# Optimization experiments

Hardware: AMD Instinct MI355X
Metric: run time of the kernel (lower is better)

Reference implementation:

```python
import jax, jax.numpy as jnp
import numpy as np
import math

B, W, BINS, BANDS = 2, 2048, 1024, 8  # cropsize == W
HEAD = BINS // BANDS


def setup_inputs() -> dict:
    key = jax.random.key(0)
    ks = jax.random.split(key, 10)
    s = 1.0 / math.sqrt(BINS)
    return {
        "x": jax.random.normal(ks[0], (B, W, BINS), jnp.float32),
        "Wq": jax.random.normal(ks[1], (BINS, BINS), jnp.float32) * s,
        "bq": jax.random.normal(ks[2], (BINS,), jnp.float32) * s,
        "Wk": jax.random.normal(ks[3], (BINS, BINS), jnp.float32) * s,
        "bk": jax.random.normal(ks[4], (BINS,), jnp.float32) * s,
        "Wv": jax.random.normal(ks[5], (BINS, BINS), jnp.float32) * s,
        "bv": jax.random.normal(ks[6], (BINS,), jnp.float32) * s,
        "Wo": jax.random.normal(ks[7], (BINS, BINS), jnp.float32) * s,
        "bo": jax.random.normal(ks[8], (BINS,), jnp.float32) * s,
        "er": jax.random.normal(ks[9], (HEAD, W), jnp.float32) * s,  # [bins//num_bands, cropsize]
    }


def reference(x, Wq, bq, Wk, bk, Wv, bv, Wo, bo, er):
    b, w, h = x.shape
    n = BANDS
    # projections -> [b, n, w, head]
    q = (x @ Wq.T + bq).reshape(b, w, n, -1).transpose(0, 2, 1, 3)
    k = (x @ Wk.T + bk).reshape(b, w, n, -1).transpose(0, 2, 1, 3)
    v = (x @ Wv.T + bv).reshape(b, w, n, -1).transpose(0, 2, 1, 3)
    # relative position bias via skew trick: [b, n, w, cropsize]
    qer = jnp.einsum('bnwd,dc->bnwc', q, er)
    p = jnp.pad(qer, ((0, 0), (0, 0), (0, 0), (1, 0)))  # pad left of last dim
    p = jnp.swapaxes(p, 2, 3)[:, :, 1:, :]              # [b, n, w, w]
    a = (jnp.einsum('bnqd,bnkd->bnqk', q, k) + p) / math.sqrt(h)
    attn = jax.nn.softmax(a, axis=-1)
    ctx = jnp.einsum('bnqk,bnkd->bnqd', attn, v).transpose(0, 2, 1, 3).reshape(b, w, h)
    o = ctx @ Wo.T + bo
    return (o, a)
```

## Files before the change

kernel.cpp:

```cpp
#include <hip/hip_runtime.h>

typedef __attribute__((ext_vector_type(8))) __bf16 bf16x8;
typedef __attribute__((ext_vector_type(4))) float f32x4;

__device__ __forceinline__ unsigned short f2bf(float f) {
  __bf16 h = (__bf16)f;
  return __builtin_bit_cast(unsigned short, h);
}

__device__ __forceinline__ f32x4 mfma_bf16(bf16x8 a, bf16x8 b, f32x4 c) {
  return __builtin_amdgcn_mfma_f32_16x16x32_bf16(a, b, c, 0, 0, 0);
}

__device__ __forceinline__ void gload_lds16(const void* g, void* l) {
  __builtin_amdgcn_global_load_lds((const __attribute__((address_space(1))) void*)g,
                                   (__attribute__((address_space(3))) void*)l, 16, 0, 0);
}


__global__ void cvt_f32_bf16(const float* __restrict__ in, unsigned short* __restrict__ out, int n4) {
  int i = blockIdx.x * blockDim.x + threadIdx.x;
  if (i < n4) {
    float4 v = reinterpret_cast<const float4*>(in)[i];
    ushort4 o;
    o.x = f2bf(v.x); o.y = f2bf(v.y); o.z = f2bf(v.z); o.w = f2bf(v.w);
    reinterpret_cast<ushort4*>(out)[i] = o;
  }
}

__global__ void cvt4_f32_bf16(const float* __restrict__ a, const float* __restrict__ b,
                              const float* __restrict__ c, const float* __restrict__ d,
                              unsigned short* __restrict__ oa, unsigned short* __restrict__ ob,
                              unsigned short* __restrict__ oc, unsigned short* __restrict__ od) {
  int i = blockIdx.x * blockDim.x + threadIdx.x;
  int which = i >> 18, j = i & 262143;
  const float* src = (which == 0) ? a : (which == 1) ? b : (which == 2) ? c : d;
  unsigned short* dst = (which == 0) ? oa : (which == 1) ? ob : (which == 2) ? oc : od;
  float4 v = reinterpret_cast<const float4*>(src)[j];
  ushort4 o;
  o.x = f2bf(v.x); o.y = f2bf(v.y); o.z = f2bf(v.z); o.w = f2bf(v.w);
  reinterpret_cast<ushort4*>(dst)[j] = o;
}

__global__ void er_transpose(const float* __restrict__ er, unsigned short* __restrict__ ert) {
  __shared__ float t[32][33];
  int w0 = blockIdx.x * 32, d0 = blockIdx.y * 32;
  int tx = threadIdx.x, ty = threadIdx.y;
#pragma unroll
  for (int i = 0; i < 4; ++i)
    t[ty + i * 8][tx] = er[(size_t)(d0 + ty + i * 8) * 2048 + w0 + tx];
  __syncthreads();
#pragma unroll
  for (int i = 0; i < 4; ++i)
    ert[(size_t)(w0 + ty + i * 8) * 128 + d0 + tx] = f2bf(t[tx][ty + i * 8]);
}


__global__ __launch_bounds__(256, 1) void gemm_qkv3(
    const unsigned short* __restrict__ xb,
    const unsigned short* __restrict__ Wqb, const unsigned short* __restrict__ Wkb,
    const unsigned short* __restrict__ Wvb,
    const float* __restrict__ bq, const float* __restrict__ bk, const float* __restrict__ bvv,
    unsigned short* __restrict__ Qb, unsigned short* __restrict__ Kb,
    unsigned short* __restrict__ Vtb)
{
  __shared__ __align__(16) char lds[131072];

  const int tid = threadIdx.x;
  const int lane = tid & 63, wid = tid >> 6;
  const int lr = lane & 15, lq = lane >> 4;
  const int wr = wid >> 1, wc = wid & 1;
  const int i0 = blockIdx.x * 128, j0 = blockIdx.y * 128;

  f32x4 aQ[4][4] = {}, aK[4][4] = {}, aV[4][4] = {};

  int ldso[4];
  const char *asrc[4], *qsrc[4], *ksrc[4], *vsrc[4];
#pragma unroll
  for (int p = 0; p < 4; ++p) {
    int L = p * 4096 + tid * 16;
    int row = L >> 7, colb = L & 127;
    int sc = colb ^ ((row & 7) << 4);
    ldso[p] = L;
    asrc[p] = (const char*)xb  + (size_t)(i0 + row) * 2048 + sc;
    qsrc[p] = (const char*)Wqb + (size_t)(j0 + row) * 2048 + sc;
    ksrc[p] = (const char*)Wkb + (size_t)(j0 + row) * 2048 + sc;
    vsrc[p] = (const char*)Wvb + (size_t)(j0 + row) * 2048 + sc;
  }

#pragma unroll
  for (int p = 0; p < 4; ++p) gload_lds16(asrc[p], lds + ldso[p]);
#pragma unroll
  for (int p = 0; p < 4; ++p) gload_lds16(qsrc[p], lds + 16384 + ldso[p]);
#pragma unroll
  for (int p = 0; p < 4; ++p) gload_lds16(ksrc[p], lds + 32768 + ldso[p]);
#pragma unroll
  for (int p = 0; p < 4; ++p) gload_lds16(vsrc[p], lds + 49152 + ldso[p]);

  const int swz = (lr & 7) << 4;

  for (int kt = 0; kt < 16; ++kt) {
    char* cb = lds + (kt & 1) * 65536;
    char* nb = lds + ((kt + 1) & 1) * 65536;

    asm volatile("s_waitcnt vmcnt(0)" ::: "memory");
    __builtin_amdgcn_sched_barrier(0);
    __builtin_amdgcn_s_barrier();
    __builtin_amdgcn_sched_barrier(0);

    if (kt < 15) {
      const int k0b = (kt + 1) * 128;
#pragma unroll
      for (int p = 0; p < 4; ++p) gload_lds16(asrc[p] + k0b, nb + ldso[p]);
#pragma unroll
      for (int p = 0; p < 4; ++p) gload_lds16(qsrc[p] + k0b, nb + 16384 + ldso[p]);
#pragma unroll
      for (int p = 0; p < 4; ++p) gload_lds16(ksrc[p] + k0b, nb + 32768 + ldso[p]);
#pragma unroll
      for (int p = 0; p < 4; ++p) gload_lds16(vsrc[p] + k0b, nb + 49152 + ldso[p]);
    }
    __builtin_amdgcn_sched_barrier(0);

#pragma unroll
    for (int kk = 0; kk < 2; ++kk) {
      const int coff = (kk * 64 + lq * 16) ^ swz;
      bf16x8 af[4];
#pragma unroll
      for (int m = 0; m < 4; ++m)
        af[m] = *(const bf16x8*)(cb + (wr * 64 + m * 16 + lr) * 128 + coff);
      bf16x8 bq_[4], bk_[4], bv_[4];
#pragma unroll
      for (int n = 0; n < 4; ++n) {
        const int rb = (wc * 64 + n * 16 + lr) * 128 + coff;
        bq_[n] = *(const bf16x8*)(cb + 16384 + rb);
        bk_[n] = *(const bf16x8*)(cb + 32768 + rb);
        bv_[n] = *(const bf16x8*)(cb + 49152 + rb);
      }
      __builtin_amdgcn_s_setprio(1);
#pragma unroll
      for (int m = 0; m < 4; ++m)
#pragma unroll
        for (int n = 0; n < 4; ++n) {
          aQ[m][n] = mfma_bf16(af[m], bq_[n], aQ[m][n]);
          aK[m][n] = mfma_bf16(af[m], bk_[n], aK[m][n]);
          aV[m][n] = mfma_bf16(af[m], bv_[n], aV[m][n]);
        }
      __builtin_amdgcn_s_setprio(0);
    }
  }

  float vbq[4], vbk[4], vbv[4];
#pragma unroll
  for (int n = 0; n < 4; ++n) {
    int gj = j0 + wc * 64 + n * 16 + lr;
    vbq[n] = bq[gj]; vbk[n] = bk[gj]; vbv[n] = bvv[gj];
  }

#pragma unroll
  for (int m = 0; m < 4; ++m)
#pragma unroll
    for (int n = 0; n < 4; ++n)
#pragma unroll
      for (int r = 0; r < 4; ++r) {
        int gi = i0 + wr * 64 + m * 16 + lq * 4 + r;
        int gj = j0 + wc * 64 + n * 16 + lr;
        Qb[(size_t)gi * 1024 + gj] = f2bf(aQ[m][n][r] + vbq[n]);
        Kb[(size_t)gi * 1024 + gj] = f2bf(aK[m][n][r] + vbk[n]);
      }

  __syncthreads();
  unsigned short* lds16 = (unsigned short*)lds;
#pragma unroll
  for (int m = 0; m < 4; ++m)
#pragma unroll
    for (int n = 0; n < 4; ++n)
#pragma unroll
      for (int r = 0; r < 4; ++r) {
        int il = wr * 64 + m * 16 + lq * 4 + r;
        int jl = wc * 64 + n * 16 + lr;
        lds16[jl * 132 + il] = f2bf(aV[m][n][r] + vbv[n]);
      }
  __syncthreads();
  {
    const int b = i0 >> 11, w0 = i0 & 2047, bd = j0 >> 7;
    for (int idx = tid; idx < 16384; idx += 256) {
      int dl = idx >> 7, wl = idx & 127;
      Vtb[(size_t)((b * 8 + bd) * 128 + dl) * 2048 + w0 + wl] = lds16[dl * 132 + wl];
    }
  }
}


__global__ __launch_bounds__(256, 2) void gemm_bt(
    const unsigned short* __restrict__ A,
    const unsigned short* __restrict__ Bt,
    const float* __restrict__ bias,
    float* __restrict__ C)
{
  __shared__ __align__(16) char base[32768];

  const int tid = threadIdx.x;
  const int lane = tid & 63, wid = tid >> 6;
  const int lr = lane & 15, lq = lane >> 4;
  const int wr = wid >> 1, wc = wid & 1;
  const int i0 = blockIdx.x * 128, j0 = blockIdx.y * 128;

  f32x4 acc[4][4] = {};

  const char* Abase = (const char*)A + (size_t)(i0 + (tid >> 2)) * 2048 + ((tid & 3) << 4);
  const char* Bbase = (const char*)Bt + (size_t)(j0 + (tid >> 2)) * 2048 + ((tid & 3) << 4);

  gload_lds16(Abase,             base + tid * 16);
  gload_lds16(Abase + 64 * 2048, base + 4096 + tid * 16);
  gload_lds16(Bbase,             base + 8192 + tid * 16);
  gload_lds16(Bbase + 64 * 2048, base + 12288 + tid * 16);

  for (int kt = 0; kt < 32; ++kt) {
    char* cbuf = base + (kt & 1) * 16384;
    char* nbuf = base + ((kt + 1) & 1) * 16384;

    asm volatile("s_waitcnt vmcnt(0)" ::: "memory");
    __builtin_amdgcn_sched_barrier(0);
    __builtin_amdgcn_s_barrier();
    __builtin_amdgcn_sched_barrier(0);

    if (kt < 31) {
      const int k0b = (kt + 1) * 64;
      gload_lds16(Abase + k0b,             nbuf + tid * 16);
      gload_lds16(Abase + k0b + 64 * 2048, nbuf + 4096 + tid * 16);
      gload_lds16(Bbase + k0b,             nbuf + 8192 + tid * 16);
      gload_lds16(Bbase + k0b + 64 * 2048, nbuf + 12288 + tid * 16);
    }
    __builtin_amdgcn_sched_barrier(0);

    bf16x8 af[4], bfr[4];
#pragma unroll
    for (int m = 0; m < 4; ++m)
      af[m] = *(const bf16x8*)(cbuf + (wr * 64 + m * 16 + lr) * 64 + lq * 16);
#pragma unroll
    for (int n = 0; n < 4; ++n)
      bfr[n] = *(const bf16x8*)(cbuf + 8192 + (wc * 64 + n * 16 + lr) * 64 + lq * 16);
    __builtin_amdgcn_s_setprio(1);
#pragma unroll
    for (int m = 0; m < 4; ++m)
#pragma unroll
      for (int n = 0; n < 4; ++n)
        acc[m][n] = mfma_bf16(af[m], bfr[n], acc[m][n]);
    __builtin_amdgcn_s_setprio(0);
  }

  float bv[4];
#pragma unroll
  for (int n = 0; n < 4; ++n) bv[n] = bias[j0 + wc * 64 + n * 16 + lr];
#pragma unroll
  for (int m = 0; m < 4; ++m)
#pragma unroll
    for (int n = 0; n < 4; ++n)
#pragma unroll
      for (int r = 0; r < 4; ++r) {
        int gi = i0 + wr * 64 + m * 16 + lq * 4 + r;
        int gj = j0 + wc * 64 + n * 16 + lr;
        C[(size_t)gi * 1024 + gj] = acc[m][n][r] + bv[n];
      }
}


__global__ __launch_bounds__(512) void attn_fused(
    const unsigned short* __restrict__ Qb,
    const unsigned short* __restrict__ Kb,
    const unsigned short* __restrict__ Vt,
    const unsigned short* __restrict__ ErT,
    float* __restrict__ a_out,
    unsigned short* __restrict__ ctx)
{
  __shared__ __align__(16) char Klb[32768];
  __shared__ __align__(16) char Qlb[32768];
  __shared__ __align__(16) char Vlb[32768];
  __shared__ __align__(16) char Plb[32768];

  const int bb = blockIdx.x;
  const int bd = bb & 7, b = bb >> 3;
  const int qi0 = blockIdx.y * 128;
  const int tid = threadIdx.x, wid = tid >> 6, lane = tid & 63;
  const int lr = lane & 15, lq = lane >> 4;

  bf16x8 qf[4], ef[4];
  {
    const unsigned short* Qrow = Qb + (size_t)(b * 2048 + qi0 + wid * 16 + lr) * 1024 + bd * 128;
    const unsigned short* Erow = ErT + (size_t)(qi0 + wid * 16 + lr) * 128;
#pragma unroll
    for (int kk = 0; kk < 4; ++kk) {
      qf[kk] = *(const bf16x8*)(Qrow + kk * 32 + lq * 8);
      ef[kk] = *(const bf16x8*)(Erow + kk * 32 + lq * 8);
    }
  }

  int ldso[4];
  const char *ksrc[4], *qsrc[4], *vsrc[4];
#pragma unroll
  for (int p = 0; p < 4; ++p) {
    int L = p * 8192 + tid * 16;
    int row = L >> 8, cs = L & 255;
    int sc = cs ^ ((row & 7) << 4);
    ldso[p] = L;
    ksrc[p] = (const char*)Kb + ((size_t)(b * 2048 + row) * 1024 + bd * 128) * 2 + sc;
    qsrc[p] = (const char*)Qb + ((size_t)(b * 2048 + row) * 1024 + bd * 128) * 2 + sc;
    vsrc[p] = (const char*)Vt + ((size_t)(bb * 128 + row) * 2048) * 2 + sc;
  }

#pragma unroll
  for (int p = 0; p < 4; ++p) gload_lds16(ksrc[p], Klb + ldso[p]);
#pragma unroll
  for (int p = 0; p < 4; ++p) gload_lds16(qsrc[p], Qlb + ldso[p]);
#pragma unroll
  for (int p = 0; p < 4; ++p) gload_lds16(vsrc[p], Vlb + ldso[p]);
  asm volatile("s_waitcnt vmcnt(0)" ::: "memory");
  __builtin_amdgcn_sched_barrier(0);

  f32x4 oacc[8] = {};
  float M[4], L[4];
#pragma unroll
  for (int r = 0; r < 4; ++r) { M[r] = -1e30f; L[r] = 0.f; }

  float* abase = a_out + (size_t)bb * 2048 * 2048;

  for (int kt = 0; kt < 16; ++kt) {
    const int kj0 = kt * 128;
    const size_t nkq = (size_t)((kt + 1) & 15) * 262144;
    const size_t nv = (size_t)((kt + 1) & 15) * 256;

    asm volatile("s_waitcnt vmcnt(36)" ::: "memory");
    __builtin_amdgcn_sched_barrier(0);
    __builtin_amdgcn_s_barrier();
    __builtin_amdgcn_sched_barrier(0);

    f32x4 sacc[8] = {};
    __builtin_amdgcn_s_setprio(1);
#pragma unroll
    for (int kk = 0; kk < 4; ++kk) {
#pragma unroll
      for (int nf = 0; nf < 8; ++nf) {
        const int row = nf * 16 + lr;
        bf16x8 kf = *(const bf16x8*)(Klb + row * 256 + ((kk * 64 + lq * 16) ^ ((row & 7) << 4)));
        sacc[nf] = mfma_bf16(qf[kk], kf, sacc[nf]);
      }
#pragma unroll
      for (int nf = 0; nf < 8; ++nf) {
        const int row = nf * 16 + lr;
        bf16x8 qkf = *(const bf16x8*)(Qlb + row * 256 + ((kk * 64 + lq * 16) ^ ((row & 7) << 4)));
        sacc[nf] = mfma_bf16(ef[kk], qkf, sacc[nf]);
      }
    }
    __builtin_amdgcn_s_setprio(0);

    __builtin_amdgcn_sched_barrier(0);
    __builtin_amdgcn_s_barrier();
    __builtin_amdgcn_sched_barrier(0);

#pragma unroll
    for (int p = 0; p < 4; ++p) gload_lds16(ksrc[p] + nkq, Klb + ldso[p]);
#pragma unroll
    for (int p = 0; p < 4; ++p) gload_lds16(qsrc[p] + nkq, Qlb + ldso[p]);
    __builtin_amdgcn_sched_barrier(0);

#pragma unroll
    for (int nf = 0; nf < 8; ++nf)
#pragma unroll
      for (int r = 0; r < 4; ++r) sacc[nf][r] *= 0.03125f;
    {
      const int qrow_base = qi0 + wid * 16 + lq * 4;
#pragma unroll
      for (int nf = 0; nf < 8; ++nf)
#pragma unroll
        for (int r = 0; r < 4; ++r)
          abase[(size_t)(qrow_base + r) * 2048 + kj0 + nf * 16 + lr] = sacc[nf][r];
    }
    __builtin_amdgcn_sched_barrier(0);

    float rmax[4];
#pragma unroll
    for (int r = 0; r < 4; ++r) {
      float m0 = sacc[0][r];
#pragma unroll
      for (int nf = 1; nf < 8; ++nf) m0 = fmaxf(m0, sacc[nf][r]);
      m0 = fmaxf(m0, __shfl_xor(m0, 1));
      m0 = fmaxf(m0, __shfl_xor(m0, 2));
      m0 = fmaxf(m0, __shfl_xor(m0, 4));
      m0 = fmaxf(m0, __shfl_xor(m0, 8));
      rmax[r] = m0;
    }
    bool small = (rmax[0] - M[0] <= 8.f) & (rmax[1] - M[1] <= 8.f) &
                 (rmax[2] - M[2] <= 8.f) & (rmax[3] - M[3] <= 8.f);
    unsigned long long vote = __ballot(small);
    if (vote != ~0ull) {
      float scl[4];
#pragma unroll
      for (int r = 0; r < 4; ++r) {
        float Mn = fmaxf(M[r], rmax[r]);
        scl[r] = __expf(M[r] - Mn);
        M[r] = Mn;
        L[r] *= scl[r];
      }
#pragma unroll
      for (int dn = 0; dn < 8; ++dn)
#pragma unroll
        for (int r = 0; r < 4; ++r) oacc[dn][r] *= scl[r];
    }
    float rsum[4] = {0.f, 0.f, 0.f, 0.f};
#pragma unroll
    for (int nf = 0; nf < 8; ++nf)
#pragma unroll
      for (int r = 0; r < 4; ++r) {
        float pv = __expf(sacc[nf][r] - M[r]);
        sacc[nf][r] = pv;
        rsum[r] += pv;
      }
    {
      const int prow0 = wid * 16 + lq * 4;
#pragma unroll
      for (int nf = 0; nf < 8; ++nf)
#pragma unroll
        for (int r = 0; r < 4; ++r) {
          const int row = prow0 + r;
          *(unsigned short*)(Plb + row * 256 + (((nf * 16 + lr) * 2) ^ ((row & 7) << 4))) =
              f2bf(sacc[nf][r]);
        }
    }
#pragma unroll
    for (int r = 0; r < 4; ++r) {
      rsum[r] += __shfl_xor(rsum[r], 1);
      rsum[r] += __shfl_xor(rsum[r], 2);
      rsum[r] += __shfl_xor(rsum[r], 4);
      rsum[r] += __shfl_xor(rsum[r], 8);
      L[r] += rsum[r];
    }

    asm volatile("s_waitcnt vmcnt(40)" ::: "memory");
    __builtin_amdgcn_sched_barrier(0);

    __builtin_amdgcn_s_setprio(1);
#pragma unroll
    for (int kk = 0; kk < 4; ++kk) {
      const int prow = wid * 16 + lr;
      bf16x8 pf = *(const bf16x8*)(Plb + prow * 256 + ((kk * 64 + lq * 16) ^ ((prow & 7) << 4)));
#pragma unroll
      for (int dn = 0; dn < 8; ++dn) {
        const int vrow = dn * 16 + lr;
        bf16x8 vf = *(const bf16x8*)(Vlb + vrow * 256 + ((kk * 64 + lq * 16) ^ ((vrow & 7) << 4)));
        oacc[dn] = mfma_bf16(pf, vf, oacc[dn]);
      }
    }
    __builtin_amdgcn_s_setprio(0);

    __builtin_amdgcn_sched_barrier(0);
    __builtin_amdgcn_s_barrier();
    __builtin_amdgcn_sched_barrier(0);
#pragma unroll
    for (int p = 0; p < 4; ++p) gload_lds16(vsrc[p] + nv, Vlb + ldso[p]);
    __builtin_amdgcn_sched_barrier(0);
  }

  {
    const int qrow_base = b * 2048 + qi0 + wid * 16 + lq * 4;
#pragma unroll
    for (int dn = 0; dn < 8; ++dn)
#pragma unroll
      for (int r = 0; r < 4; ++r) {
        float v = oacc[dn][r] / L[r];
        ctx[(size_t)(qrow_base + r) * 1024 + bd * 128 + dn * 16 + lr] = f2bf(v);
      }
  }
}


extern "C" void kernel_launch(void* const* d_in, const int* in_sizes, int n_in,
                              void* d_out, int out_size, void* d_ws, size_t ws_size,
                              hipStream_t stream) {
  const float* x  = (const float*)d_in[0];
  const float* Wq = (const float*)d_in[1];
  const float* bq = (const float*)d_in[2];
  const float* Wk = (const float*)d_in[3];
  const float* bk = (const float*)d_in[4];
  const float* Wv = (const float*)d_in[5];
  const float* bv = (const float*)d_in[6];
  const float* Wo = (const float*)d_in[7];
  const float* bo = (const float*)d_in[8];
  const float* er = (const float*)d_in[9];

  char* ws = (char*)d_ws;
  unsigned short* xb  = (unsigned short*)(ws + 0);
  unsigned short* Wqb = (unsigned short*)(ws + 8388608);
  unsigned short* Wkb = (unsigned short*)(ws + 10485760);
  unsigned short* Wvb = (unsigned short*)(ws + 12582912);
  unsigned short* Wob = (unsigned short*)(ws + 14680064);
  unsigned short* Qb  = (unsigned short*)(ws + 16777216);
  unsigned short* Kb  = (unsigned short*)(ws + 25165824);
  unsigned short* Vtb = (unsigned short*)(ws + 33554432);
  unsigned short* ctx = (unsigned short*)(ws + 41943040);
  unsigned short* ert = (unsigned short*)(ws + 50331648);

  float* a_out = (float*)d_out + 4194304;

  cvt_f32_bf16<<<dim3(4096), dim3(256), 0, stream>>>(x, xb, 1048576);
  cvt4_f32_bf16<<<dim3(4096), dim3(256), 0, stream>>>(Wq, Wk, Wv, Wo, Wqb, Wkb, Wvb, Wob);
  er_transpose<<<dim3(64, 4), dim3(32, 8), 0, stream>>>(er, ert);

  gemm_qkv3<<<dim3(32, 8), dim3(256), 0, stream>>>(xb, Wqb, Wkb, Wvb, bq, bk, bv,
                                                   Qb, Kb, Vtb);

  attn_fused<<<dim3(16, 16), dim3(512), 0, stream>>>(Qb, Kb, Vtb, ert, a_out, ctx);

  gemm_bt<<<dim3(32, 8), dim3(256), 0, stream>>>(ctx, Wob, bo, (float*)d_out);
}
```

Before: 183.5 us.

## Split attention tile into 2x2 warp grid with cross-wave softmax reduction

Each wave now covers 32 query rows by 64 key columns instead of 16 rows by 128 columns. Every K, Q-skew and V fragment read from LDS then feeds two MFMAs, which halves per-wave LDS fragment reads. Row max and row sum are combined across the two column waves through small shared arrays. This adds an extra block barrier per key tile, plus a shared-memory round trip for the max and the sum.

```diff
diff --git a/kernel.cpp b/kernel.cpp
--- a/kernel.cpp
+++ b/kernel.cpp
@@ -277,21 +277,26 @@
   __shared__ __align__(16) char Qlb[32768];
   __shared__ __align__(16) char Vlb[32768];
   __shared__ __align__(16) char Plb[32768];
+  __shared__ float Xm[128][2];
+  __shared__ float Xs[128][2];
 
   const int bb = blockIdx.x;
   const int bd = bb & 7, b = bb >> 3;
   const int qi0 = blockIdx.y * 128;
   const int tid = threadIdx.x, wid = tid >> 6, lane = tid & 63;
   const int lr = lane & 15, lq = lane >> 4;
-
-  bf16x8 qf[4], ef[4];
-  {
-    const unsigned short* Qrow = Qb + (size_t)(b * 2048 + qi0 + wid * 16 + lr) * 1024 + bd * 128;
-    const unsigned short* Erow = ErT + (size_t)(qi0 + wid * 16 + lr) * 128;
+  const int wr = wid >> 1, wc = wid & 1;
+
+  bf16x8 qf[2][4], ef[2][4];
+#pragma unroll
+  for (int fr = 0; fr < 2; ++fr) {
+    const unsigned short* Qrow =
+        Qb + (size_t)(b * 2048 + qi0 + wr * 32 + fr * 16 + lr) * 1024 + bd * 128;
+    const unsigned short* Erow = ErT + (size_t)(qi0 + wr * 32 + fr * 16 + lr) * 128;
 #pragma unroll
     for (int kk = 0; kk < 4; ++kk) {
-      qf[kk] = *(const bf16x8*)(Qrow + kk * 32 + lq * 8);
-      ef[kk] = *(const bf16x8*)(Erow + kk * 32 + lq * 8);
+      qf[fr][kk] = *(const bf16x8*)(Qrow + kk * 32 + lq * 8);
+      ef[fr][kk] = *(const bf16x8*)(Erow + kk * 32 + lq * 8);
     }
   }
 
@@ -317,10 +322,12 @@
   asm volatile("s_waitcnt vmcnt(0)" ::: "memory");
   __builtin_amdgcn_sched_barrier(0);
 
-  f32x4 oacc[8] = {};
-  float M[4], L[4];
-#pragma unroll
-  for (int r = 0; r < 4; ++r) { M[r] = -1e30f; L[r] = 0.f; }
+  f32x4 oacc[2][4] = {};
+  float M[2][4], Ls[2][4];
+#pragma unroll
+  for (int fr = 0; fr < 2; ++fr)
+#pragma unroll
+    for (int r = 0; r < 4; ++r) { M[fr][r] = -1e30f; Ls[fr][r] = 0.f; }
 
   float* abase = a_out + (size_t)bb * 2048 * 2048;
 
@@ -334,21 +341,20 @@
     __builtin_amdgcn_s_barrier();
     __builtin_amdgcn_sched_barrier(0);
 
-    f32x4 sacc[8] = {};
+    f32x4 sacc[2][4] = {};
     __builtin_amdgcn_s_setprio(1);
 #pragma unroll
     for (int kk = 0; kk < 4; ++kk) {
 #pragma unroll
-      for (int nf = 0; nf < 8; ++nf) {
-        const int row = nf * 16 + lr;
-        bf16x8 kf = *(const bf16x8*)(Klb + row * 256 + ((kk * 64 + lq * 16) ^ ((row & 7) << 4)));
-        sacc[nf] = mfma_bf16(qf[kk], kf, sacc[nf]);
-      }
-#pragma unroll
-      for (int nf = 0; nf < 8; ++nf) {
-        const int row = nf * 16 + lr;
-        bf16x8 qkf = *(const bf16x8*)(Qlb + row * 256 + ((kk * 64 + lq * 16) ^ ((row & 7) << 4)));
-        sacc[nf] = mfma_bf16(ef[kk], qkf, sacc[nf]);
+      for (int nf = 0; nf < 4; ++nf) {
+        const int row = wc * 64 + nf * 16 + lr;
+        const int coff = (kk * 64 + lq * 16) ^ ((row & 7) << 4);
+        bf16x8 kf = *(const bf16x8*)(Klb + row * 256 + coff);
+        sacc[0][nf] = mfma_bf16(qf[0][kk], kf, sacc[0][nf]);
+        sacc[1][nf] = mfma_bf16(qf[1][kk], kf, sacc[1][nf]);
+        bf16x8 qkf = *(const bf16x8*)(Qlb + row * 256 + coff);
+        sacc[0][nf] = mfma_bf16(ef[0][kk], qkf, sacc[0][nf]);
+        sacc[1][nf] = mfma_bf16(ef[1][kk], qkf, sacc[1][nf]);
       }
     }
     __builtin_amdgcn_s_setprio(0);
@@ -364,90 +370,122 @@
     __builtin_amdgcn_sched_barrier(0);
 
 #pragma unroll
-    for (int nf = 0; nf < 8; ++nf)
-#pragma unroll
-      for (int r = 0; r < 4; ++r) sacc[nf][r] *= 0.03125f;
-    {
-      const int qrow_base = qi0 + wid * 16 + lq * 4;
-#pragma unroll
-      for (int nf = 0; nf < 8; ++nf)
+    for (int fr = 0; fr < 2; ++fr) {
+#pragma unroll
+      for (int nf = 0; nf < 4; ++nf)
+#pragma unroll
+        for (int r = 0; r < 4; ++r) sacc[fr][nf][r] *= 0.03125f;
+      const int qrow_base = qi0 + wr * 32 + fr * 16 + lq * 4;
+#pragma unroll
+      for (int nf = 0; nf < 4; ++nf)
 #pragma unroll
         for (int r = 0; r < 4; ++r)
-          abase[(size_t)(qrow_base + r) * 2048 + kj0 + nf * 16 + lr] = sacc[nf][r];
-    }
-    __builtin_amdgcn_sched_barrier(0);
-
-    float rmax[4];
-#pragma unroll
-    for (int r = 0; r < 4; ++r) {
-      float m0 = sacc[0][r];
-#pragma unroll
-      for (int nf = 1; nf < 8; ++nf) m0 = fmaxf(m0, sacc[nf][r]);
-      m0 = fmaxf(m0, __shfl_xor(m0, 1));
-      m0 = fmaxf(m0, __shfl_xor(m0, 2));
-      m0 = fmaxf(m0, __shfl_xor(m0, 4));
-      m0 = fmaxf(m0, __shfl_xor(m0, 8));
-      rmax[r] = m0;
-    }
-    bool small = (rmax[0] - M[0] <= 8.f) & (rmax[1] - M[1] <= 8.f) &
-                 (rmax[2] - M[2] <= 8.f) & (rmax[3] - M[3] <= 8.f);
+          abase[(size_t)(qrow_base + r) * 2048 + kj0 + wc * 64 + nf * 16 + lr] =
+              sacc[fr][nf][r];
+    }
+    __builtin_amdgcn_sched_barrier(0);
+
+    float rmax[2][4];
+#pragma unroll
+    for (int fr = 0; fr < 2; ++fr)
+#pragma unroll
+      for (int r = 0; r < 4; ++r) {
+        float m0 = fmaxf(fmaxf(sacc[fr][0][r], sacc[fr][1][r]),
+                         fmaxf(sacc[fr][2][r], sacc[fr][3][r]));
+        m0 = fmaxf(m0, __shfl_xor(m0, 1));
+        m0 = fmaxf(m0, __shfl_xor(m0, 2));
+        m0 = fmaxf(m0, __shfl_xor(m0, 4));
+        m0 = fmaxf(m0, __shfl_xor(m0, 8));
+        rmax[fr][r] = m0;
+        if (lr == 0) Xm[wr * 32 + fr * 16 + lq * 4 + r][wc] = m0;
+      }
+    __builtin_amdgcn_s_barrier();
+#pragma unroll
+    for (int fr = 0; fr < 2; ++fr)
+#pragma unroll
+      for (int r = 0; r < 4; ++r)
+        rmax[fr][r] = fmaxf(rmax[fr][r], Xm[wr * 32 + fr * 16 + lq * 4 + r][wc ^ 1]);
+
+    bool small = true;
+#pragma unroll
+    for (int fr = 0; fr < 2; ++fr)
+#pragma unroll
+      for (int r = 0; r < 4; ++r) small &= (rmax[fr][r] - M[fr][r] <= 8.f);
     unsigned long long vote = __ballot(small);
     if (vote != ~0ull) {
-      float scl[4];
-#pragma unroll
-      for (int r = 0; r < 4; ++r) {
-        float Mn = fmaxf(M[r], rmax[r]);
-        scl[r] = __expf(M[r] - Mn);
-        M[r] = Mn;
-        L[r] *= scl[r];
-      }
-#pragma unroll
-      for (int dn = 0; dn < 8; ++dn)
-#pragma unroll
-        for (int r = 0; r < 4; ++r) oacc[dn][r] *= scl[r];
-    }
-    float rsum[4] = {0.f, 0.f, 0.f, 0.f};
-#pragma unroll
-    for (int nf = 0; nf < 8; ++nf)
-#pragma unroll
-      for (int r = 0; r < 4; ++r) {
-        float pv = __expf(sacc[nf][r] - M[r]);
-        sacc[nf][r] = pv;
-        rsum[r] += pv;
-      }
-    {
-      const int prow0 = wid * 16 + lq * 4;
-#pragma unroll
-      for (int nf = 0; nf < 8; ++nf)
+#pragma unroll
+      for (int fr = 0; fr < 2; ++fr) {
+        float scl[4];
+#pragma unroll
+        for (int r = 0; r < 4; ++r) {
+          float Mn = fmaxf(M[fr][r], rmax[fr][r]);
+          scl[r] = __expf(M[fr][r] - Mn);
+          M[fr][r] = Mn;
+          Ls[fr][r] *= scl[r];
+        }
+#pragma unroll
+        for (int dn = 0; dn < 4; ++dn)
+#pragma unroll
+          for (int r = 0; r < 4; ++r) oacc[fr][dn][r] *= scl[r];
+      }
+    }
+
+    float rsum[2][4];
+#pragma unroll
+    for (int fr = 0; fr < 2; ++fr) {
+#pragma unroll
+      for (int r = 0; r < 4; ++r) rsum[fr][r] = 0.f;
+#pragma unroll
+      for (int nf = 0; nf < 4; ++nf)
+#pragma unroll
+        for (int r = 0; r < 4; ++r) {
+          float pv = __expf(sacc[fr][nf][r] - M[fr][r]);
+          sacc[fr][nf][r] = pv;
+          rsum[fr][r] += pv;
+        }
+      const int prow0 = wr * 32 + fr * 16 + lq * 4;
+#pragma unroll
+      for (int nf = 0; nf < 4; ++nf)
 #pragma unroll
         for (int r = 0; r < 4; ++r) {
           const int row = prow0 + r;
-          *(unsigned short*)(Plb + row * 256 + (((nf * 16 + lr) * 2) ^ ((row & 7) << 4))) =
-              f2bf(sacc[nf][r]);
+          *(unsigned short*)(Plb + row * 256 +
+              (((wc * 64 + nf * 16 + lr) * 2) ^ ((row & 7) << 4))) = f2bf(sacc[fr][nf][r]);
         }
-    }
-#pragma unroll
-    for (int r = 0; r < 4; ++r) {
-      rsum[r] += __shfl_xor(rsum[r], 1);
-      rsum[r] += __shfl_xor(rsum[r], 2);
-      rsum[r] += __shfl_xor(rsum[r], 4);
-      rsum[r] += __shfl_xor(rsum[r], 8);
-      L[r] += rsum[r];
+#pragma unroll
+      for (int r = 0; r < 4; ++r) {
+        rsum[fr][r] += __shfl_xor(rsum[fr][r], 1);
+        rsum[fr][r] += __shfl_xor(rsum[fr][r], 2);
+        rsum[fr][r] += __shfl_xor(rsum[fr][r], 4);
+        rsum[fr][r] += __shfl_xor(rsum[fr][r], 8);
+        if (lr == 0) Xs[prow0 + r][wc] = rsum[fr][r];
+      }
     }
 
     asm volatile("s_waitcnt vmcnt(40)" ::: "memory");
     __builtin_amdgcn_sched_barrier(0);
+    __builtin_amdgcn_s_barrier();
+    __builtin_amdgcn_sched_barrier(0);
+
+#pragma unroll
+    for (int fr = 0; fr < 2; ++fr)
+#pragma unroll
+      for (int r = 0; r < 4; ++r)
+        Ls[fr][r] += rsum[fr][r] + Xs[wr * 32 + fr * 16 + lq * 4 + r][wc ^ 1];
 
     __builtin_amdgcn_s_setprio(1);
 #pragma unroll
     for (int kk = 0; kk < 4; ++kk) {
-      const int prow = wid * 16 + lr;
-      bf16x8 pf = *(const bf16x8*)(Plb + prow * 256 + ((kk * 64 + lq * 16) ^ ((prow & 7) << 4)));
-#pragma unroll
-      for (int dn = 0; dn < 8; ++dn) {
-        const int vrow = dn * 16 + lr;
+      const int pr0 = wr * 32 + lr;
+      const int pr1 = pr0 + 16;
+      bf16x8 pf0 = *(const bf16x8*)(Plb + pr0 * 256 + ((kk * 64 + lq * 16) ^ ((pr0 & 7) << 4)));
+      bf16x8 pf1 = *(const bf16x8*)(Plb + pr1 * 256 + ((kk * 64 + lq * 16) ^ ((pr1 & 7) << 4)));
+#pragma unroll
+      for (int dn = 0; dn < 4; ++dn) {
+        const int vrow = wc * 64 + dn * 16 + lr;
         bf16x8 vf = *(const bf16x8*)(Vlb + vrow * 256 + ((kk * 64 + lq * 16) ^ ((vrow & 7) << 4)));
-        oacc[dn] = mfma_bf16(pf, vf, oacc[dn]);
+        oacc[0][dn] = mfma_bf16(pf0, vf, oacc[0][dn]);
+        oacc[1][dn] = mfma_bf16(pf1, vf, oacc[1][dn]);
       }
     }
     __builtin_amdgcn_s_setprio(0);
@@ -460,14 +498,15 @@
     __builtin_amdgcn_sched_barrier(0);
   }
 
-  {
-    const int qrow_base = b * 2048 + qi0 + wid * 16 + lq * 4;
-#pragma unroll
-    for (int dn = 0; dn < 8; ++dn)
+#pragma unroll
+  for (int fr = 0; fr < 2; ++fr) {
+    const int qrow_base = b * 2048 + qi0 + wr * 32 + fr * 16 + lq * 4;
+#pragma unroll
+    for (int dn = 0; dn < 4; ++dn)
 #pragma unroll
       for (int r = 0; r < 4; ++r) {
-        float v = oacc[dn][r] / L[r];
-        ctx[(size_t)(qrow_base + r) * 1024 + bd * 128 + dn * 16 + lr] = f2bf(v);
+        float v = oacc[fr][dn][r] / Ls[fr][r];
+        ctx[(size_t)(qrow_base + r) * 1024 + bd * 128 + wc * 64 + dn * 16 + lr] = f2bf(v);
       }
   }
 }
```

New measurement: 211.6 us. 1.15x slower.
